# Optimization experiments

Hardware: AMD Instinct MI355X
Metric: run time of the kernel (lower is better)

## Reference

```python
import jax, jax.numpy as jnp
import numpy as np

NX, NY = 4096, 4096
DX, DY, DT = 1e-3, 1e-3, 5e-4


def setup_inputs() -> dict:
    key = jax.random.key(0)
    k1, k2, k3, k4 = jax.random.split(key, 4)
    shp = (1, 1, NX, NY)
    return {
        "Ez": jax.random.normal(k1, shp, dtype=jnp.float32),
        "Hx": jax.random.normal(k2, shp, dtype=jnp.float32),
        "Hy": jax.random.normal(k3, shp, dtype=jnp.float32),
        "eps": jnp.ones(shp, dtype=jnp.float32),
        "mu": jnp.ones(shp, dtype=jnp.float32),
        "sigma": jax.random.uniform(k4, shp, dtype=jnp.float32),
    }


def _ddx(f, inv2dx):
    # central difference along axis 0, zero on all boundary cells
    # (matches the sparse stencil which is only populated for interior rows)
    d = jnp.zeros_like(f)
    return d.at[1:-1, 1:-1].set((f[2:, 1:-1] - f[:-2, 1:-1]) * inv2dx)


def _ddy(f, inv2dy):
    d = jnp.zeros_like(f)
    return d.at[1:-1, 1:-1].set((f[1:-1, 2:] - f[1:-1, :-2]) * inv2dy)


def reference(Ez, Hx, Hy, eps, mu, sigma):
    ez = Ez[0, 0]
    hx = Hx[0, 0]
    hy = Hy[0, 0]
    eps2 = eps[0, 0]
    mu2 = mu[0, 0]
    sig2 = sigma[0, 0]
    inv2dx = 1.0 / (2.0 * DX)
    inv2dy = 1.0 / (2.0 * DY)

    # H updates from curl of Ez
    hx_new = hx - DT * (_ddy(ez, inv2dy) / mu2)
    hy_new = hy + DT * (_ddx(ez, inv2dx) / mu2)

    # Ez update from curl of H (lossy medium semi-implicit coefficients)
    curl_z = _ddx(hy_new, inv2dx) - _ddy(hx_new, inv2dy)
    A_plus = 1.0 + sig2 * DT / (2.0 * eps2)
    A_minus = 1.0 - sig2 * DT / (2.0 * eps2)
    ez_new = (A_minus / A_plus) * ez + (DT / (A_plus * eps2)) * curl_z

    shp = (1, 1, NX, NY)
    return (ez_new.reshape(shp), hx_new.reshape(shp), hy_new.reshape(shp))
```

## Files before the change

### kernel.cpp

```cpp
#include <hip/hip_runtime.h>

#define NXg 4096
#define NYg 4096

typedef float v4f __attribute__((ext_vector_type(4)));

__global__ __launch_bounds__(256) void fdtd_step_kernel(
    const float* __restrict__ ez, const float* __restrict__ hx,
    const float* __restrict__ hy, const float* __restrict__ eps,
    const float* __restrict__ mu, const float* __restrict__ sigma,
    float* __restrict__ ez_out, float* __restrict__ hx_out,
    float* __restrict__ hy_out)
{
    const int j0 = (blockIdx.x * blockDim.x + threadIdx.x) * 4;
    const int i  = blockIdx.y;
    const long row = (long)i * NYg;
    const long idx = row + j0;

    constexpr float DT = 5e-4f;
    constexpr float inv2dx = 500.0f;
    constexpr float inv2dy = 500.0f;

    const bool iin = (i >= 1) && (i < NXg - 1);
    const bool iP2 = (i < NXg - 2);
    const bool iM2 = (i >= 2);

    const int rm1 = (i >= 1) ? i - 1 : i;
    const int rp1 = (i < NXg - 1) ? i + 1 : i;
    const int rm2 = (i >= 2) ? i - 2 : i;
    const int rp2 = (i < NXg - 2) ? i + 2 : i;

    const long jm = (j0 == 0) ? (long)j0 : (long)j0 - 4;
    const long jp = (j0 == NYg - 4) ? (long)j0 : (long)j0 + 4;

    const v4f ezL  = *(const v4f*)(ez + row + jm);
    const v4f ezC4 = *(const v4f*)(ez + idx);
    const v4f ezR  = *(const v4f*)(ez + row + jp);
    const v4f ezU  = *(const v4f*)(ez + (long)rp1 * NYg + j0);
    const v4f ezD  = *(const v4f*)(ez + (long)rm1 * NYg + j0);
    const v4f ezU2 = *(const v4f*)(ez + (long)rp2 * NYg + j0);
    const v4f ezD2 = *(const v4f*)(ez + (long)rm2 * NYg + j0);

    const v4f hxL  = *(const v4f*)(hx + row + jm);
    const v4f hxC4 = *(const v4f*)(hx + idx);
    const v4f hxR  = *(const v4f*)(hx + row + jp);

    const v4f hyC4 = *(const v4f*)(hy + idx);
    const v4f hyU  = *(const v4f*)(hy + (long)rp1 * NYg + j0);
    const v4f hyD  = *(const v4f*)(hy + (long)rm1 * NYg + j0);

    const v4f muL  = *(const v4f*)(mu + row + jm);
    const v4f muC4 = *(const v4f*)(mu + idx);
    const v4f muR  = *(const v4f*)(mu + row + jp);
    const v4f muU  = *(const v4f*)(mu + (long)rp1 * NYg + j0);
    const v4f muD  = *(const v4f*)(mu + (long)rm1 * NYg + j0);

    const v4f ep4  = *(const v4f*)(eps + idx);
    const v4f sg4  = *(const v4f*)(sigma + idx);

    float ezw[12], hxw[12], muw[12];
    *(v4f*)&ezw[0] = ezL;  *(v4f*)&ezw[4] = ezC4;  *(v4f*)&ezw[8] = ezR;
    *(v4f*)&hxw[0] = hxL;  *(v4f*)&hxw[4] = hxC4;  *(v4f*)&hxw[8] = hxR;
    *(v4f*)&muw[0] = muL;  *(v4f*)&muw[4] = muC4;  *(v4f*)&muw[8] = muR;

    v4f ezo, hxo, hyo;

#pragma unroll
    for (int e = 0; e < 4; ++e) {
        const int j = j0 + e;
        const bool jin = (j >= 1) && (j < NYg - 1);
        const bool interior = iin && jin;

        const float ezCv  = ezw[e + 4];
        const float invmu = __builtin_amdgcn_rcpf(muw[e + 4]);

        const float ddy = interior ? (ezw[e + 5] - ezw[e + 3]) * inv2dy : 0.0f;
        const float ddx = interior ? (ezU[e] - ezD[e]) * inv2dx : 0.0f;

        const float hx_new = hxw[e + 4] - DT * ddy * invmu;
        const float hy_new = hyC4[e]    + DT * ddx * invmu;

        float curl = 0.0f;
        if (interior) {
            const float dExP = iP2 ? (ezU2[e] - ezCv) * inv2dx : 0.0f;
            const float dExM = iM2 ? (ezCv - ezD2[e]) * inv2dx : 0.0f;
            const float hyP = hyU[e] + DT * dExP * __builtin_amdgcn_rcpf(muU[e]);
            const float hyM = hyD[e] + DT * dExM * __builtin_amdgcn_rcpf(muD[e]);

            const float dEyP = (j < NYg - 2) ? (ezw[e + 6] - ezCv) * inv2dy : 0.0f;
            const float dEyM = (j >= 2)      ? (ezCv - ezw[e + 2]) * inv2dy : 0.0f;
            const float hxP = hxw[e + 5] - DT * dEyP * __builtin_amdgcn_rcpf(muw[e + 5]);
            const float hxM = hxw[e + 3] - DT * dEyM * __builtin_amdgcn_rcpf(muw[e + 3]);

            curl = (hyP - hyM) * inv2dx - (hxP - hxM) * inv2dy;
        }

        const float ep  = ep4[e];
        const float rep = __builtin_amdgcn_rcpf(ep);
        const float s   = sg4[e] * DT * 0.5f * rep;
        const float Ap  = 1.0f + s;
        const float Am  = 1.0f - s;
        const float rAp = __builtin_amdgcn_rcpf(Ap);

        ezo[e] = Am * rAp * ezCv + DT * rAp * rep * curl;
        hxo[e] = hx_new;
        hyo[e] = hy_new;
    }

    __builtin_nontemporal_store(ezo, (v4f*)(ez_out + idx));
    __builtin_nontemporal_store(hxo, (v4f*)(hx_out + idx));
    __builtin_nontemporal_store(hyo, (v4f*)(hy_out + idx));
}

extern "C" void kernel_launch(void* const* d_in, const int* in_sizes, int n_in,
                              void* d_out, int out_size, void* d_ws, size_t ws_size,
                              hipStream_t stream) {
    const float* ez    = (const float*)d_in[0];
    const float* hx    = (const float*)d_in[1];
    const float* hy    = (const float*)d_in[2];
    const float* eps   = (const float*)d_in[3];
    const float* mu    = (const float*)d_in[4];
    const float* sigma = (const float*)d_in[5];

    const long N = (long)NXg * NYg;
    float* out    = (float*)d_out;
    float* ez_out = out;
    float* hx_out = out + N;
    float* hy_out = out + 2 * N;

    dim3 block(256, 1, 1);
    dim3 grid(NYg / (256 * 4), NXg, 1);
    fdtd_step_kernel<<<grid, block, 0, stream>>>(ez, hx, hy, eps, mu, sigma,
                                                 ez_out, hx_out, hy_out);
}
```

Baseline: 465.0 us.

## Process eight rows per thread with rolling register window for vertical stencil

Each thread now walks RROWS consecutive rows, keeping the vertical ez/mu/hy neighbours in a rolling register window so each row is loaded once instead of several times. Eps and sigma are read with nontemporal loads. The grid shrinks by the row-block factor, which lowers parallelism and occupancy, and the per-row loads inside the loop serialize somewhat.

New measurement: 472.2 us. Within noise of the previous version (+1.5%).

```diff
diff --git a/kernel.cpp b/kernel.cpp
--- a/kernel.cpp
+++ b/kernel.cpp
@@ -2,8 +2,11 @@
 
 #define NXg 4096
 #define NYg 4096
+#define RROWS 8
 
 typedef float v4f __attribute__((ext_vector_type(4)));
+
+__device__ __forceinline__ v4f ldv(const float* p) { return *(const v4f*)p; }
 
 __global__ __launch_bounds__(256) void fdtd_step_kernel(
     const float* __restrict__ ez, const float* __restrict__ hx,
@@ -13,103 +16,110 @@
     float* __restrict__ hy_out)
 {
     const int j0 = (blockIdx.x * blockDim.x + threadIdx.x) * 4;
-    const int i  = blockIdx.y;
-    const long row = (long)i * NYg;
-    const long idx = row + j0;
+    const int i0 = blockIdx.y * RROWS;
 
     constexpr float DT = 5e-4f;
     constexpr float inv2dx = 500.0f;
     constexpr float inv2dy = 500.0f;
 
-    const bool iin = (i >= 1) && (i < NXg - 1);
-    const bool iP2 = (i < NXg - 2);
-    const bool iM2 = (i >= 2);
-
-    const int rm1 = (i >= 1) ? i - 1 : i;
-    const int rp1 = (i < NXg - 1) ? i + 1 : i;
-    const int rm2 = (i >= 2) ? i - 2 : i;
-    const int rp2 = (i < NXg - 2) ? i + 2 : i;
-
     const long jm = (j0 == 0) ? (long)j0 : (long)j0 - 4;
     const long jp = (j0 == NYg - 4) ? (long)j0 : (long)j0 + 4;
 
-    const v4f ezL  = *(const v4f*)(ez + row + jm);
-    const v4f ezC4 = *(const v4f*)(ez + idx);
-    const v4f ezR  = *(const v4f*)(ez + row + jp);
-    const v4f ezU  = *(const v4f*)(ez + (long)rp1 * NYg + j0);
-    const v4f ezD  = *(const v4f*)(ez + (long)rm1 * NYg + j0);
-    const v4f ezU2 = *(const v4f*)(ez + (long)rp2 * NYg + j0);
-    const v4f ezD2 = *(const v4f*)(ez + (long)rm2 * NYg + j0);
+    auto rowb = [](int r) -> long {
+        r = r < 0 ? 0 : (r > NXg - 1 ? NXg - 1 : r);
+        return (long)r * NYg;
+    };
 
-    const v4f hxL  = *(const v4f*)(hx + row + jm);
-    const v4f hxC4 = *(const v4f*)(hx + idx);
-    const v4f hxR  = *(const v4f*)(hx + row + jp);
-
-    const v4f hyC4 = *(const v4f*)(hy + idx);
-    const v4f hyU  = *(const v4f*)(hy + (long)rp1 * NYg + j0);
-    const v4f hyD  = *(const v4f*)(hy + (long)rm1 * NYg + j0);
-
-    const v4f muL  = *(const v4f*)(mu + row + jm);
-    const v4f muC4 = *(const v4f*)(mu + idx);
-    const v4f muR  = *(const v4f*)(mu + row + jp);
-    const v4f muU  = *(const v4f*)(mu + (long)rp1 * NYg + j0);
-    const v4f muD  = *(const v4f*)(mu + (long)rm1 * NYg + j0);
-
-    const v4f ep4  = *(const v4f*)(eps + idx);
-    const v4f sg4  = *(const v4f*)(sigma + idx);
-
-    float ezw[12], hxw[12], muw[12];
-    *(v4f*)&ezw[0] = ezL;  *(v4f*)&ezw[4] = ezC4;  *(v4f*)&ezw[8] = ezR;
-    *(v4f*)&hxw[0] = hxL;  *(v4f*)&hxw[4] = hxC4;  *(v4f*)&hxw[8] = hxR;
-    *(v4f*)&muw[0] = muL;  *(v4f*)&muw[4] = muC4;  *(v4f*)&muw[8] = muR;
-
-    v4f ezo, hxo, hyo;
+    v4f ezm2 = ldv(ez + rowb(i0 - 2) + j0);
+    v4f ezm1 = ldv(ez + rowb(i0 - 1) + j0);
+    v4f ezc  = ldv(ez + rowb(i0)     + j0);
+    v4f ezp1 = ldv(ez + rowb(i0 + 1) + j0);
+    v4f mum1 = ldv(mu + rowb(i0 - 1) + j0);
+    v4f muc  = ldv(mu + rowb(i0)     + j0);
+    v4f hym1 = ldv(hy + rowb(i0 - 1) + j0);
+    v4f hyc  = ldv(hy + rowb(i0)     + j0);
 
 #pragma unroll
-    for (int e = 0; e < 4; ++e) {
-        const int j = j0 + e;
-        const bool jin = (j >= 1) && (j < NYg - 1);
-        const bool interior = iin && jin;
+    for (int s = 0; s < RROWS; ++s) {
+        const int i = i0 + s;
+        const long row = (long)i * NYg;
+        const long idx = row + j0;
 
-        const float ezCv  = ezw[e + 4];
-        const float invmu = __builtin_amdgcn_rcpf(muw[e + 4]);
+        const v4f ezp2 = ldv(ez + rowb(i + 2) + j0);
+        const v4f mup1 = ldv(mu + rowb(i + 1) + j0);
+        const v4f hyp1 = ldv(hy + rowb(i + 1) + j0);
 
-        const float ddy = interior ? (ezw[e + 5] - ezw[e + 3]) * inv2dy : 0.0f;
-        const float ddx = interior ? (ezU[e] - ezD[e]) * inv2dx : 0.0f;
+        const v4f ezL = ldv(ez + row + jm);
+        const v4f ezR = ldv(ez + row + jp);
+        const v4f muL = ldv(mu + row + jm);
+        const v4f muR = ldv(mu + row + jp);
+        const v4f hxL = ldv(hx + row + jm);
+        const v4f hxC = ldv(hx + idx);
+        const v4f hxR = ldv(hx + row + jp);
+        const v4f ep4 = __builtin_nontemporal_load((const v4f*)(eps + idx));
+        const v4f sg4 = __builtin_nontemporal_load((const v4f*)(sigma + idx));
 
-        const float hx_new = hxw[e + 4] - DT * ddy * invmu;
-        const float hy_new = hyC4[e]    + DT * ddx * invmu;
+        const bool iin = (i >= 1) && (i < NXg - 1);
+        const bool iP2 = (i < NXg - 2);
+        const bool iM2 = (i >= 2);
 
-        float curl = 0.0f;
-        if (interior) {
-            const float dExP = iP2 ? (ezU2[e] - ezCv) * inv2dx : 0.0f;
-            const float dExM = iM2 ? (ezCv - ezD2[e]) * inv2dx : 0.0f;
-            const float hyP = hyU[e] + DT * dExP * __builtin_amdgcn_rcpf(muU[e]);
-            const float hyM = hyD[e] + DT * dExM * __builtin_amdgcn_rcpf(muD[e]);
+        float ezw[12], hxw[12], muw[12];
+        *(v4f*)&ezw[0] = ezL; *(v4f*)&ezw[4] = ezc; *(v4f*)&ezw[8] = ezR;
+        *(v4f*)&hxw[0] = hxL; *(v4f*)&hxw[4] = hxC; *(v4f*)&hxw[8] = hxR;
+        *(v4f*)&muw[0] = muL; *(v4f*)&muw[4] = muc; *(v4f*)&muw[8] = muR;
 
-            const float dEyP = (j < NYg - 2) ? (ezw[e + 6] - ezCv) * inv2dy : 0.0f;
-            const float dEyM = (j >= 2)      ? (ezCv - ezw[e + 2]) * inv2dy : 0.0f;
-            const float hxP = hxw[e + 5] - DT * dEyP * __builtin_amdgcn_rcpf(muw[e + 5]);
-            const float hxM = hxw[e + 3] - DT * dEyM * __builtin_amdgcn_rcpf(muw[e + 3]);
+        v4f ezo, hxo, hyo;
 
-            curl = (hyP - hyM) * inv2dx - (hxP - hxM) * inv2dy;
+#pragma unroll
+        for (int e = 0; e < 4; ++e) {
+            const int j = j0 + e;
+            const bool jin = (j >= 1) && (j < NYg - 1);
+            const bool interior = iin && jin;
+
+            const float ezCv  = ezw[e + 4];
+            const float invmu = __builtin_amdgcn_rcpf(muw[e + 4]);
+
+            const float ddy = interior ? (ezw[e + 5] - ezw[e + 3]) * inv2dy : 0.0f;
+            const float ddx = interior ? (ezp1[e] - ezm1[e]) * inv2dx : 0.0f;
+
+            const float hx_new = hxw[e + 4] - DT * ddy * invmu;
+            const float hy_new = hyc[e]     + DT * ddx * invmu;
+
+            float curl = 0.0f;
+            if (interior) {
+                const float dExP = iP2 ? (ezp2[e] - ezCv) * inv2dx : 0.0f;
+                const float dExM = iM2 ? (ezCv - ezm2[e]) * inv2dx : 0.0f;
+                const float hyP = hyp1[e] + DT * dExP * __builtin_amdgcn_rcpf(mup1[e]);
+                const float hyM = hym1[e] + DT * dExM * __builtin_amdgcn_rcpf(mum1[e]);
+
+                const float dEyP = (j < NYg - 2) ? (ezw[e + 6] - ezCv) * inv2dy : 0.0f;
+                const float dEyM = (j >= 2)      ? (ezCv - ezw[e + 2]) * inv2dy : 0.0f;
+                const float hxP = hxw[e + 5] - DT * dEyP * __builtin_amdgcn_rcpf(muw[e + 5]);
+                const float hxM = hxw[e + 3] - DT * dEyM * __builtin_amdgcn_rcpf(muw[e + 3]);
+
+                curl = (hyP - hyM) * inv2dx - (hxP - hxM) * inv2dy;
+            }
+
+            const float ep  = ep4[e];
+            const float rep = __builtin_amdgcn_rcpf(ep);
+            const float sv  = sg4[e] * DT * 0.5f * rep;
+            const float Ap  = 1.0f + sv;
+            const float Am  = 1.0f - sv;
+            const float rAp = __builtin_amdgcn_rcpf(Ap);
+
+            ezo[e] = Am * rAp * ezCv + DT * rAp * rep * curl;
+            hxo[e] = hx_new;
+            hyo[e] = hy_new;
         }
 
-        const float ep  = ep4[e];
-        const float rep = __builtin_amdgcn_rcpf(ep);
-        const float s   = sg4[e] * DT * 0.5f * rep;
-        const float Ap  = 1.0f + s;
-        const float Am  = 1.0f - s;
-        const float rAp = __builtin_amdgcn_rcpf(Ap);
+        __builtin_nontemporal_store(ezo, (v4f*)(ez_out + idx));
+        __builtin_nontemporal_store(hxo, (v4f*)(hx_out + idx));
+        __builtin_nontemporal_store(hyo, (v4f*)(hy_out + idx));
 
-        ezo[e] = Am * rAp * ezCv + DT * rAp * rep * curl;
-        hxo[e] = hx_new;
-        hyo[e] = hy_new;
+        ezm2 = ezm1; ezm1 = ezc; ezc = ezp1; ezp1 = ezp2;
+        mum1 = muc;  muc = mup1;
+        hym1 = hyc;  hyc = hyp1;
     }
-
-    __builtin_nontemporal_store(ezo, (v4f*)(ez_out + idx));
-    __builtin_nontemporal_store(hxo, (v4f*)(hx_out + idx));
-    __builtin_nontemporal_store(hyo, (v4f*)(hy_out + idx));
 }
 
 extern "C" void kernel_launch(void* const* d_in, const int* in_sizes, int n_in,
@@ -129,7 +139,7 @@
     float* hy_out = out + 2 * N;
 
     dim3 block(256, 1, 1);
-    dim3 grid(NYg / (256 * 4), NXg, 1);
+    dim3 grid(NYg / (256 * 4), NXg / RROWS, 1);
     fdtd_step_kernel<<<grid, block, 0, stream>>>(ez, hx, hy, eps, mu, sigma,
                                                  ez_out, hx_out, hy_out);
 }
```
